# Kernel optimization log

Hardware: AMD Instinct MI355X
Metric: run time of the kernel (lower is better)

## Reference

```python
import jax, jax.numpy as jnp
import numpy as np

N = 10000
E = 256000
MUL = 32            # multiplicity per l (hidden_sizes = [32]*4)
NB = 10             # nbasis_funcs
RMAX = 3.5          # max_radius
NAVG = 25.6         # navg_neighbors
NGRAPH = 16         # number of graphs in batch
SLICES = [(0, 1), (1, 4), (4, 9), (9, 16)]  # l=0..3 blocks of the 16-dim SH rep


def _sph_harm(u):
    """Real spherical harmonics l=0..3, component normalization, on unit vectors. [E,16]"""
    x, y, z = u[:, 0], u[:, 1], u[:, 2]
    one = jnp.ones_like(x)
    s3 = 3.0 ** 0.5
    s15 = 15.0 ** 0.5
    s5 = 5.0 ** 0.5
    a = (35.0 / 8.0) ** 0.5
    b = 105.0 ** 0.5
    c = (21.0 / 8.0) ** 0.5
    d = 7.0 ** 0.5 / 2.0
    cols = [
        one,
        s3 * x, s3 * y, s3 * z,
        s15 * x * y, s15 * y * z, 0.5 * s5 * (3 * z * z - 1), s15 * x * z, 0.5 * s15 * (x * x - y * y),
        a * y * (3 * x * x - y * y), b * x * y * z, c * y * (5 * z * z - 1), d * z * (5 * z * z - 3),
        c * x * (5 * z * z - 1), 0.5 * b * z * (x * x - y * y), a * x * (x * x - 3 * y * y),
    ]
    return jnp.stack(cols, axis=1)


def _radial(emb, W1, W2):
    # FullyConnectedNet-style MLP with fan-in normalization and silu
    h = jax.nn.silu(emb @ W1 / (NB ** 0.5))
    return h @ W2 / (W1.shape[1] ** 0.5)


def _edge_geometry(pos, edge_src, edge_dst):
    vec = pos[edge_src] - pos[edge_dst]          # [E,3]
    r = jnp.linalg.norm(vec, axis=1)             # [E]
    u = vec / (r[:, None] + 1e-9)
    sh = _sph_harm(u)                            # [E,16]
    t = jnp.clip(r / RMAX, 0.0, 1.0)
    cutoff = jnp.where(r < RMAX, 0.5 * (jnp.cos(jnp.pi * t) + 1.0), 0.0)
    edge_attr = cutoff[:, None] * sh             # [E,16]
    centers = jnp.linspace(0.0, RMAX, NB)
    step = RMAX / (NB - 1)
    emb = jnp.exp(-(((r[:, None] - centers) / step) ** 2)) / 1.12 * (NB ** 0.5)
    return edge_attr, emb


def _layer(feat, edge_src, edge_dst, edge_attr, emb, Wsc, Wr1, Wr2):
    """Gated interaction block: self-connection + per-edge radial-weighted TP conv + gate."""
    n = feat.shape[0]
    # self-connection: per-l channel mixing
    sc = jnp.concatenate(
        [jnp.einsum('nci,co->noi', feat[:, :, a:b], Wsc[l]) for l, (a, b) in enumerate(SLICES)],
        axis=2) / (MUL ** 0.5)
    # per-edge weights from radial MLP: [E, 2 paths, 4 l's, MUL]
    w = _radial(emb, Wr1, Wr2).reshape(-1, 2, 4, MUL)
    xs = feat[edge_src]                          # [E,MUL,16] gather
    # path A (0e x Yl -> l) for l=0, plus path B (l x Yl -> 0e) for l=1..3 -> scalar slot
    scal = w[:, 0, 0, :] * xs[:, :, 0] * edge_attr[:, 0:1]
    parts = []
    for l, (a, b) in enumerate(SLICES):
        if l == 0:
            continue
        scal = scal + w[:, 1, l, :] * jnp.einsum('eci,ei->ec', xs[:, :, a:b], edge_attr[:, a:b])
        parts.append(w[:, 0, l, :, None] * xs[:, :, 0:1] * edge_attr[:, None, a:b])
    msg = jnp.concatenate([scal[:, :, None]] + parts, axis=2)   # [E,MUL,16]
    agg = jax.ops.segment_sum(msg, edge_dst, num_segments=n) / (NAVG ** 0.5)
    y = sc + agg
    # equivariant gate: silu on scalars, sigmoid(scalar) gates l>0 features
    s = y[:, :, 0]
    return jnp.concatenate(
        [jax.nn.silu(s)[:, :, None], y[:, :, 1:] * jax.nn.sigmoid(s)[:, :, None]], axis=2)


def _forward(pos, x, batch, edge_src, edge_dst, W_sc, Wr1, Wr2, Wf1, Wf2):
    n = pos.shape[0]
    edge_attr, emb = _edge_geometry(pos, edge_src, edge_dst)
    # lift scalar input features into the full l=0..3 layout
    feat = jnp.zeros((n, MUL, 16), x.dtype).at[:, :, 0].set(x)
    for i in range(3):
        feat = _layer(feat, edge_src, edge_dst, edge_attr, emb, W_sc[i], Wr1[i], Wr2[i])
    # final interaction block -> 1x0e output per node
    wf = _radial(emb, Wf1, Wf2).reshape(-1, 4, MUL)             # [E,4,MUL]
    xs = feat[edge_src]
    ms = wf[:, 0, :] * xs[:, :, 0] * edge_attr[:, 0:1]
    for l, (a, b) in enumerate(SLICES):
        if l == 0:
            continue
        ms = ms + wf[:, l, :] * jnp.einsum('eci,ei->ec', xs[:, :, a:b], edge_attr[:, a:b])
    node = jax.ops.segment_sum(ms.sum(axis=1) / (MUL ** 0.5), edge_dst, num_segments=n) / (NAVG ** 0.5)
    out = jax.ops.segment_sum(node, batch, num_segments=NGRAPH) / (NAVG ** 0.5)
    return out.flatten()


def setup_inputs() -> dict:
    key = jax.random.key(0)
    ks = jax.random.split(key, 10)
    pos = jax.random.uniform(ks[0], (N, 3), jnp.float32) * 5.0
    x = jax.random.normal(ks[1], (N, MUL), jnp.float32)
    batch = jnp.sort(jax.random.randint(ks[2], (N,), 0, NGRAPH, jnp.int32))
    edge_src = jax.random.randint(ks[3], (E,), 0, N, jnp.int32)
    edge_dst = jax.random.randint(ks[4], (E,), 0, N, jnp.int32)
    W_sc = jax.random.normal(ks[5], (3, 4, MUL, MUL), jnp.float32)
    Wr1 = jax.random.normal(ks[6], (3, NB, 64), jnp.float32)
    Wr2 = jax.random.normal(ks[7], (3, 64, 2 * 4 * MUL), jnp.float32)
    Wf1 = jax.random.normal(ks[8], (NB, 64), jnp.float32)
    Wf2 = jax.random.normal(ks[9], (64, 4 * MUL), jnp.float32)
    return {"pos": pos, "x": x, "batch": batch, "edge_src": edge_src, "edge_dst": edge_dst,
            "W_sc": W_sc, "Wr1": Wr1, "Wr2": Wr2, "Wf1": Wf1, "Wf2": Wf2}


def reference(pos, x, batch, edge_src, edge_dst, W_sc, Wr1, Wr2, Wf1, Wf2):
    return _forward(pos, x, batch, edge_src, edge_dst, W_sc, Wr1, Wr2, Wf1, Wf2)
```

## Files before the change

kernel.cpp:

```cpp
#include <hip/hip_runtime.h>
#include <math.h>

#define NN 10000
#define EE 256000
#define NGR 16
#define ECAP 150016

#define RSQRT10F   0.31622776601683794f
#define EMB_SCALE  2.8234621965789103f
#define INV_SQRT_MUL  0.17677669529663687f
#define INV_SQRT_NAVG 0.19764235376052372f
#define SCREC      (0.125f * INV_SQRT_NAVG)
#define STEPF      0.3888888888888889f
#define INV_STEPF  2.5714285714285716f
#define PIF        3.14159265358979323846f

__device__ __forceinline__ float sigm(float x) {
    return 1.0f / (1.0f + __expf(-x));
}

__device__ __forceinline__ void atomAddF(float* p, float v) {
    __hip_atomic_fetch_add(p, v, __ATOMIC_RELAXED, __HIP_MEMORY_SCOPE_AGENT);
}

__global__ __launch_bounds__(256) void count_kernel(
    const float* __restrict__ pos, const int* __restrict__ esrc,
    const int* __restrict__ edst, int* __restrict__ deg)
{
    int e = blockIdx.x * 256 + threadIdx.x;
    if (e >= EE) return;
    int s = esrc[e], d = edst[e];
    float vx = pos[3*s+0] - pos[3*d+0];
    float vy = pos[3*s+1] - pos[3*d+1];
    float vz = pos[3*s+2] - pos[3*d+2];
    float r2 = vx*vx + vy*vy + vz*vz;
    if (r2 < 12.25f) atomicAdd(&deg[d], 1);
}

__global__ __launch_bounds__(256) void scan_kernel(
    const int* __restrict__ deg, int* __restrict__ off, int* __restrict__ cursor)
{
    __shared__ int sbuf[256];
    const int t = threadIdx.x;
    const int start = t * 40;
    const int end = (start + 40 < NN) ? start + 40 : NN;
    int s = 0;
    for (int i = start; i < end; ++i) s += deg[i];
    sbuf[t] = s;
    __syncthreads();
    for (int d = 1; d < 256; d <<= 1) {
        int v = (t >= d) ? sbuf[t - d] : 0;
        __syncthreads();
        sbuf[t] += v;
        __syncthreads();
    }
    int run = sbuf[t] - s;
    for (int i = start; i < end; ++i) {
        off[i] = run; cursor[i] = run; run += deg[i];
    }
    if (t == 255) off[NN] = sbuf[255];
}

__global__ __launch_bounds__(256) void w1t_kernel(
    const float* __restrict__ Wr1, const float* __restrict__ Wf1,
    float* __restrict__ w1t)
{
    int t = blockIdx.x * 256 + threadIdx.x;
    if (t >= 4096) return;
    int i = t & 15;
    int j = (t >> 4) & 63;
    int l = t >> 10;
    float v;
    if (l < 3) v = (i < 10) ? Wr1[l * 640 + i * 64 + j] : 0.0f;
    else       v = (i < 10) ? Wf1[i * 64 + j] : 0.0f;
    w1t[l * 1024 + j * 16 + i] = v;
}

__global__ __launch_bounds__(256) void pack_kernel(
    const float* __restrict__ Wr2, const float* __restrict__ Wf2,
    float* __restrict__ wr2p, float* __restrict__ wf2p)
{
    const int offs[7] = {0, 32, 64, 96, 160, 192, 224};
    int t = blockIdx.x * 256 + threadIdx.x;
    if (t < 49152) {
        int k = t & 63;
        int j = (t >> 6) & 63;
        int g = (t >> 12) & 3;
        int layer = t >> 14;
        float v = 0.0f;
        if (k < 56)
            v = Wr2[layer * 16384 + j * 256 + offs[k >> 3] + g * 8 + (k & 7)];
        wr2p[t] = v;
    } else if (t < 49152 + 8192) {
        int t2 = t - 49152;
        int u = t2 & 15;
        int l = (t2 >> 4) & 3;
        int j = (t2 >> 6) & 63;
        int g = t2 >> 12;
        wf2p[t2] = Wf2[j * 128 + l * 32 + g * 16 + u];
    }
}

__global__ __launch_bounds__(256) void scatter_kernel(
    const float* __restrict__ pos, const int* __restrict__ esrc,
    const int* __restrict__ edst, int* __restrict__ cursor,
    int* __restrict__ csrc, int* __restrict__ cdst,
    float* __restrict__ attr_soa, float* __restrict__ attr_e,
    float* __restrict__ emb_soa)
{
    int e = blockIdx.x * 256 + threadIdx.x;
    if (e >= EE) return;
    int s = esrc[e], d = edst[e];
    float vx = pos[3*s+0] - pos[3*d+0];
    float vy = pos[3*s+1] - pos[3*d+1];
    float vz = pos[3*s+2] - pos[3*d+2];
    float r2 = vx*vx + vy*vy + vz*vz;
    if (r2 >= 12.25f) return;
    float r = sqrtf(r2);
    int slot = atomicAdd(&cursor[d], 1);
    if (slot >= ECAP) return;

    float inv = 1.0f / (r + 1e-9f);
    float x = vx * inv, y = vy * inv, z = vz * inv;

    float t = r * (1.0f / 3.5f);
    float cw = 0.5f * (cosf(PIF * t) + 1.0f);

    const float s3  = 1.7320508075688772f;
    const float s15 = 3.872983346207417f;
    const float s5  = 2.23606797749979f;
    const float a4  = 2.0916500663351889f;
    const float b4  = 10.246950765959598f;
    const float c4  = 1.6201851746019651f;
    const float d4  = 1.3228756555322954f;
    float xx = x*x, yy = y*y, zz = z*z;
    float sh[16];
    sh[0]  = 1.0f;
    sh[1]  = s3 * x;
    sh[2]  = s3 * y;
    sh[3]  = s3 * z;
    sh[4]  = s15 * x * y;
    sh[5]  = s15 * y * z;
    sh[6]  = 0.5f * s5 * (3.0f*zz - 1.0f);
    sh[7]  = s15 * x * z;
    sh[8]  = 0.5f * s15 * (xx - yy);
    sh[9]  = a4 * y * (3.0f*xx - yy);
    sh[10] = b4 * x * y * z;
    sh[11] = c4 * y * (5.0f*zz - 1.0f);
    sh[12] = d4 * z * (5.0f*zz - 3.0f);
    sh[13] = c4 * x * (5.0f*zz - 1.0f);
    sh[14] = 0.5f * b4 * z * (xx - yy);
    sh[15] = a4 * x * (xx - 3.0f*yy);

    float4* ae = (float4*)(attr_e + (size_t)slot * 16);
    #pragma unroll
    for (int q = 0; q < 4; ++q)
        ae[q] = make_float4(cw*sh[q*4], cw*sh[q*4+1], cw*sh[q*4+2], cw*sh[q*4+3]);

    #pragma unroll
    for (int i = 0; i < 16; ++i)
        attr_soa[(size_t)i * ECAP + slot] = cw * sh[i];
    #pragma unroll
    for (int k = 0; k < 10; ++k) {
        float dd = (r - (float)k * STEPF) * INV_STEPF;
        emb_soa[(size_t)k * ECAP + slot] = __expf(-dd * dd) * EMB_SCALE;
    }
    csrc[slot] = s;
    cdst[slot] = d;
}

__global__ __launch_bounds__(256) void init_feat_kernel(
    const float* __restrict__ x, float* __restrict__ feat)
{
    int t = blockIdx.x * 256 + threadIdx.x;
    if (t >= NN * 512) return;
    int i = t & 15;
    int c = (t >> 4) & 31;
    int n = t >> 9;
    feat[t] = (i == 0) ? x[n * 32 + c] : 0.0f;
}

__global__ __launch_bounds__(256) void h_kernel(
    const float* __restrict__ w1t, const float* __restrict__ emb_soa,
    float* __restrict__ h_soa, const int* __restrict__ cntp)
{
    const int tid = threadIdx.x;
    int cnt = *cntp; if (cnt > ECAP) cnt = ECAP;
    if (cnt == 0) return;
    const int e = blockIdx.x * 256 + tid;
    if (blockIdx.x * 256 >= cnt) return;
    const bool alive = (e < cnt);
    const int ee = alive ? e : (cnt - 1);

    float emb[10];
    #pragma unroll
    for (int i = 0; i < 10; ++i)
        emb[i] = emb_soa[(size_t)i * ECAP + ee];

    #pragma unroll 4
    for (int j = 0; j < 64; ++j) {
        const float* wj = w1t + j * 16;
        float a = 0.0f;
        #pragma unroll
        for (int i = 0; i < 10; ++i)
            a += emb[i] * wj[i];
        a *= RSQRT10F;
        if (alive)
            h_soa[(size_t)j * ECAP + e] = a * sigm(a);
    }
}

__global__ __launch_bounds__(256, 4) void edge_mlp_kernel(
    const float* __restrict__ wr2p, const float* __restrict__ h_soa,
    const float* __restrict__ fin, float* __restrict__ rec,
    const int* __restrict__ csrc,
    const float* __restrict__ attr_soa, const int* __restrict__ cntp)
{
    const int tid = threadIdx.x;
    const int g = blockIdx.y;
    const int c0 = g * 8;
    int cnt = *cntp; if (cnt > ECAP) cnt = ECAP;
    if (cnt == 0) return;
    const int e = blockIdx.x * 256 + tid;
    if (blockIdx.x * 256 >= cnt) return;
    const bool alive = (e < cnt);
    const int ee = alive ? e : (cnt - 1);

    float attr[16];
    #pragma unroll
    for (int i = 0; i < 16; ++i)
        attr[i] = attr_soa[(size_t)i * ECAP + ee];

    const float* xb = fin + (size_t)csrc[ee] * 512;
    const float* hp = h_soa + ee;
    const float* wg = wr2p + (size_t)g * 4096;
    float4* rec4 = (float4*)rec;

    float a0[8], a1[8], a2[8], a3[8], a4[8], a5[8], a6[8];
    #pragma unroll
    for (int u = 0; u < 8; ++u) {
        a0[u] = 0.f; a1[u] = 0.f; a2[u] = 0.f; a3[u] = 0.f;
        a4[u] = 0.f; a5[u] = 0.f; a6[u] = 0.f;
    }
    #pragma unroll 4
    for (int j = 0; j < 64; ++j) {
        const float hj = hp[(size_t)j * ECAP];
        const float* w = wg + j * 64;
        #pragma unroll
        for (int u = 0; u < 8; ++u) {
            a0[u] += hj * w[u];
            a1[u] += hj * w[8 + u];
            a2[u] += hj * w[16 + u];
            a3[u] += hj * w[24 + u];
            a4[u] += hj * w[32 + u];
            a5[u] += hj * w[40 + u];
            a6[u] += hj * w[48 + u];
        }
    }
    #pragma unroll
    for (int u = 0; u < 8; ++u) {
        const int c = c0 + u;
        const float4* xv = (const float4*)(xb + c * 16);
        float4 x0 = xv[0], x1 = xv[1], x2 = xv[2], x3 = xv[3];
        float d1 = x0.y*attr[1] + x0.z*attr[2] + x0.w*attr[3];
        float d2 = x1.x*attr[4] + x1.y*attr[5] + x1.z*attr[6]
                 + x1.w*attr[7] + x2.x*attr[8];
        float d3 = x2.y*attr[9] + x2.z*attr[10] + x2.w*attr[11]
                 + x3.x*attr[12] + x3.y*attr[13] + x3.z*attr[14]
                 + x3.w*attr[15];
        const float xs0 = x0.x;
        float scal = SCREC * (a0[u]*xs0*attr[0] + a4[u]*d1 + a5[u]*d2 + a6[u]*d3);
        float px = SCREC * xs0;
        if (alive)
            rec4[(size_t)c * ECAP + e] =
                make_float4(scal, a1[u] * px, a2[u] * px, a3[u] * px);
    }
}

__global__ __launch_bounds__(256) void agg_kernel(
    const float* __restrict__ fin, float* __restrict__ fout,
    const float* __restrict__ Wsc, const float* __restrict__ rec,
    const float* __restrict__ attr_e, const int* __restrict__ off)
{
    int t = blockIdx.x * 256 + threadIdx.x;
    int c = t & 31;
    int n = t >> 5;
    if (n >= NN) return;

    float acc[16];
    #pragma unroll
    for (int i = 0; i < 16; ++i) acc[i] = 0.0f;

    const float* f = fin + (size_t)n * 512;
    for (int cin = 0; cin < 32; ++cin) {
        float w0 = Wsc[          cin * 32 + c];
        float w1 = Wsc[1024 + cin * 32 + c];
        float w2 = Wsc[2048 + cin * 32 + c];
        float w3 = Wsc[3072 + cin * 32 + c];
        const float4* fv = (const float4*)(f + cin * 16);
        float4 f0 = fv[0], f1 = fv[1], f2 = fv[2], f3 = fv[3];
        acc[0]  += f0.x * w0;
        acc[1]  += f0.y * w1; acc[2]  += f0.z * w1; acc[3]  += f0.w * w1;
        acc[4]  += f1.x * w2; acc[5]  += f1.y * w2; acc[6]  += f1.z * w2;
        acc[7]  += f1.w * w2; acc[8]  += f2.x * w2;
        acc[9]  += f2.y * w3; acc[10] += f2.z * w3; acc[11] += f2.w * w3;
        acc[12] += f3.x * w3; acc[13] += f3.y * w3; acc[14] += f3.z * w3;
        acc[15] += f3.w * w3;
    }
    #pragma unroll
    for (int i = 0; i < 16; ++i) acc[i] *= INV_SQRT_MUL;

    const float4* rec4 = (const float4*)rec;
    int e0 = off[n], e1 = off[n + 1];
    if (e1 > ECAP) e1 = ECAP;
    for (int e = e0; e < e1; ++e) {
        float4 v = rec4[(size_t)c * ECAP + e];
        const float4* av = (const float4*)(attr_e + (size_t)e * 16);
        float4 A0 = av[0], A1 = av[1], A2 = av[2], A3 = av[3];
        acc[0]  += v.x;
        acc[1]  += v.y * A0.y;
        acc[2]  += v.y * A0.z;
        acc[3]  += v.y * A0.w;
        acc[4]  += v.z * A1.x;
        acc[5]  += v.z * A1.y;
        acc[6]  += v.z * A1.z;
        acc[7]  += v.z * A1.w;
        acc[8]  += v.z * A2.x;
        acc[9]  += v.w * A2.y;
        acc[10] += v.w * A2.z;
        acc[11] += v.w * A2.w;
        acc[12] += v.w * A3.x;
        acc[13] += v.w * A3.y;
        acc[14] += v.w * A3.z;
        acc[15] += v.w * A3.w;
    }

    float s = acc[0];
    float g = sigm(s);
    float4 o0 = make_float4(s * g,      acc[1] * g,  acc[2] * g,  acc[3] * g);
    float4 o1 = make_float4(acc[4] * g, acc[5] * g,  acc[6] * g,  acc[7] * g);
    float4 o2 = make_float4(acc[8] * g, acc[9] * g,  acc[10] * g, acc[11] * g);
    float4 o3 = make_float4(acc[12] * g, acc[13] * g, acc[14] * g, acc[15] * g);
    float4* ov = (float4*)(fout + (size_t)n * 512 + c * 16);
    ov[0] = o0; ov[1] = o1; ov[2] = o2; ov[3] = o3;
}

__global__ __launch_bounds__(256, 2) void final_edge_kernel(
    const float* __restrict__ wf2p, const float* __restrict__ h_soa,
    const float* __restrict__ fin, float* __restrict__ fbuf,
    const int* __restrict__ csrc,
    const float* __restrict__ attr_soa, const int* __restrict__ cntp)
{
    const int tid = threadIdx.x;
    const int g = blockIdx.y;
    const int c0 = g * 16;
    int cnt = *cntp; if (cnt > ECAP) cnt = ECAP;
    if (cnt == 0) return;
    const int e = blockIdx.x * 256 + tid;
    if (blockIdx.x * 256 >= cnt) return;
    const bool alive = (e < cnt);
    const int ee = alive ? e : (cnt - 1);

    float attr[16];
    #pragma unroll
    for (int i = 0; i < 16; ++i)
        attr[i] = attr_soa[(size_t)i * ECAP + ee];

    const float* hp = h_soa + ee;
    const float* wg = wf2p + (size_t)g * 4096;
    float H0[16], H1[16], H2[16], H3[16];
    #pragma unroll
    for (int u = 0; u < 16; ++u) { H0[u]=0.f; H1[u]=0.f; H2[u]=0.f; H3[u]=0.f; }
    #pragma unroll 2
    for (int j = 0; j < 64; ++j) {
        const float hj = hp[(size_t)j * ECAP];
        const float* w = wg + j * 64;
        #pragma unroll
        for (int u = 0; u < 16; ++u) {
            H0[u] += hj * w[u];
            H1[u] += hj * w[16 + u];
            H2[u] += hj * w[32 + u];
            H3[u] += hj * w[48 + u];
        }
    }

    const float* xb = fin + (size_t)csrc[ee] * 512;
    float msum = 0.0f;
    #pragma unroll 2
    for (int u = 0; u < 16; ++u) {
        const float4* xv = (const float4*)(xb + (c0 + u) * 16);
        float4 x0 = xv[0], x1 = xv[1], x2 = xv[2], x3 = xv[3];
        float d0 = x0.x * attr[0];
        float d1 = x0.y*attr[1] + x0.z*attr[2] + x0.w*attr[3];
        float d2 = x1.x*attr[4] + x1.y*attr[5] + x1.z*attr[6]
                 + x1.w*attr[7] + x2.x*attr[8];
        float d3 = x2.y*attr[9] + x2.z*attr[10] + x2.w*attr[11]
                 + x3.x*attr[12] + x3.y*attr[13] + x3.z*attr[14]
                 + x3.w*attr[15];
        msum += H0[u]*d0 + H1[u]*d1 + H2[u]*d2 + H3[u]*d3;
    }

    if (alive)
        fbuf[(size_t)g * ECAP + e] = msum * 0.125f;
}

__global__ __launch_bounds__(256) void out_kernel(
    const float* __restrict__ fbuf, const int* __restrict__ off,
    const int* __restrict__ batch, float* __restrict__ out)
{
    __shared__ float bins[NGR];
    int t = blockIdx.x * 256 + threadIdx.x;
    if (threadIdx.x < NGR) bins[threadIdx.x] = 0.0f;
    __syncthreads();
    if (t < NN) {
        int e0 = off[t], e1 = off[t + 1];
        if (e1 > ECAP) e1 = ECAP;
        float s = 0.0f;
        for (int e = e0; e < e1; ++e)
            s += fbuf[e] + fbuf[(size_t)ECAP + e];
        atomicAdd(&bins[batch[t]], s * (INV_SQRT_MUL * (1.0f / 25.6f)));
    }
    __syncthreads();
    if (threadIdx.x < NGR) atomAddF(out + threadIdx.x, bins[threadIdx.x]);
}

extern "C" void kernel_launch(void* const* d_in, const int* in_sizes, int n_in,
                              void* d_out, int out_size, void* d_ws, size_t ws_size,
                              hipStream_t stream)
{
    const float* pos  = (const float*)d_in[0];
    const float* x    = (const float*)d_in[1];
    const int*   batch= (const int*)  d_in[2];
    const int*   esrc = (const int*)  d_in[3];
    const int*   edst = (const int*)  d_in[4];
    const float* W_sc = (const float*)d_in[5];
    const float* Wr1  = (const float*)d_in[6];
    const float* Wr2  = (const float*)d_in[7];
    const float* Wf1  = (const float*)d_in[8];
    const float* Wf2  = (const float*)d_in[9];
    float* out = (float*)d_out;

    char* ws = (char*)d_ws;
    size_t off_b = 0;
    auto alloc = [&](size_t bytes) -> void* {
        void* p = ws + off_b;
        off_b = (off_b + bytes + 255) & ~(size_t)255;
        return p;
    };
    int*   deg      = (int*)  alloc((size_t)NN * 4);
    int*   off      = (int*)  alloc((size_t)(NN + 1) * 4);
    int*   cursor   = (int*)  alloc((size_t)NN * 4);
    int*   csrc     = (int*)  alloc((size_t)ECAP * 4);
    int*   cdst     = (int*)  alloc((size_t)ECAP * 4);
    float* w1t      = (float*)alloc((size_t)4 * 1024 * 4);
    float* wr2p     = (float*)alloc((size_t)3 * 16384 * 4);
    float* wf2p     = (float*)alloc((size_t)8192 * 4);
    float* emb_soa  = (float*)alloc((size_t)10 * ECAP * 4);
    float* attr_soa = (float*)alloc((size_t)16 * ECAP * 4);
    float* attr_e   = (float*)alloc((size_t)16 * ECAP * 4);
    float* h_soa    = (float*)alloc((size_t)64 * ECAP * 4);
    float* rec      = (float*)alloc((size_t)128 * ECAP * 4);
    float* feat_a   = (float*)alloc((size_t)NN * 512 * 4);
    float* feat_b   = (float*)alloc((size_t)NN * 512 * 4);

    hipMemsetAsync(deg, 0, (size_t)NN * 4, stream);
    hipMemsetAsync(d_out, 0, (size_t)out_size * 4, stream);

    count_kernel<<<(EE + 255) / 256, 256, 0, stream>>>(pos, esrc, edst, deg);
    scan_kernel<<<1, 256, 0, stream>>>(deg, off, cursor);
    w1t_kernel<<<16, 256, 0, stream>>>(Wr1, Wf1, w1t);
    pack_kernel<<<(49152 + 8192 + 255) / 256, 256, 0, stream>>>(
        Wr2, Wf2, wr2p, wf2p);
    scatter_kernel<<<(EE + 255) / 256, 256, 0, stream>>>(
        pos, esrc, edst, cursor, csrc, cdst, attr_soa, attr_e, emb_soa);
    init_feat_kernel<<<(NN * 512 + 255) / 256, 256, 0, stream>>>(x, feat_a);

    const int* cntp = off + NN;
    float* fin = feat_a;
    float* fout = feat_b;
    dim3 egrid(ECAP / 256, 4);
    for (int layer = 0; layer < 3; ++layer) {
        h_kernel<<<ECAP / 256, 256, 0, stream>>>(
            w1t + layer * 1024, emb_soa, h_soa, cntp);
        edge_mlp_kernel<<<egrid, 256, 0, stream>>>(
            wr2p + (size_t)layer * 16384, h_soa, fin, rec,
            csrc, attr_soa, cntp);
        agg_kernel<<<(NN * 32 + 255) / 256, 256, 0, stream>>>(
            fin, fout, W_sc + layer * 4096, rec, attr_e, off);
        float* tmp = fin; fin = fout; fout = tmp;
    }
    h_kernel<<<ECAP / 256, 256, 0, stream>>>(
        w1t + 3 * 1024, emb_soa, h_soa, cntp);
    float* fbuf = rec;
    final_edge_kernel<<<dim3(ECAP / 256, 2), 256, 0, stream>>>(
        wf2p, h_soa, fin, fbuf, csrc, attr_soa, cntp);
    out_kernel<<<(NN + 255) / 256, 256, 0, stream>>>(fbuf, off, batch, out);
}
```

Before: 838.0 us.

## Store radial hidden per edge as rows and loop channel groups in one thread

The hidden activations h move from a structure-of-arrays layout to an edge-major layout of 64 floats per edge. h_kernel now writes each edge's values as float4 chunks, and the MLP kernels read them back with float4 loads. edge_mlp_kernel drops its 4-way blockIdx.y split over channel groups and loops over the 4 groups inside each thread, so h and attr are loaded once per edge instead of once per group. In exchange the grid has 4x fewer blocks and launch bounds drop to 2 blocks per CU. The per-thread float4 row reads are strided by 256 bytes, which makes loads less coalesced than the old SoA layout.

```diff
diff --git a/kernel.cpp b/kernel.cpp
--- a/kernel.cpp
+++ b/kernel.cpp
@@ -182,7 +182,7 @@
 
 __global__ __launch_bounds__(256) void h_kernel(
     const float* __restrict__ w1t, const float* __restrict__ emb_soa,
-    float* __restrict__ h_soa, const int* __restrict__ cntp)
+    float* __restrict__ h_e, const int* __restrict__ cntp)
 {
     const int tid = threadIdx.x;
     int cnt = *cntp; if (cnt > ECAP) cnt = ECAP;
@@ -197,28 +197,33 @@
     for (int i = 0; i < 10; ++i)
         emb[i] = emb_soa[(size_t)i * ECAP + ee];
 
+    float4* hrow = (float4*)(h_e + (size_t)e * 64);
     #pragma unroll 4
-    for (int j = 0; j < 64; ++j) {
-        const float* wj = w1t + j * 16;
-        float a = 0.0f;
+    for (int jb = 0; jb < 16; ++jb) {
+        float hv[4];
         #pragma unroll
-        for (int i = 0; i < 10; ++i)
-            a += emb[i] * wj[i];
-        a *= RSQRT10F;
+        for (int q = 0; q < 4; ++q) {
+            const int j = jb * 4 + q;
+            const float* wj = w1t + j * 16;
+            float a = 0.0f;
+            #pragma unroll
+            for (int i = 0; i < 10; ++i)
+                a += emb[i] * wj[i];
+            a *= RSQRT10F;
+            hv[q] = a * sigm(a);
+        }
         if (alive)
-            h_soa[(size_t)j * ECAP + e] = a * sigm(a);
-    }
-}
-
-__global__ __launch_bounds__(256, 4) void edge_mlp_kernel(
-    const float* __restrict__ wr2p, const float* __restrict__ h_soa,
+            hrow[jb] = make_float4(hv[0], hv[1], hv[2], hv[3]);
+    }
+}
+
+__global__ __launch_bounds__(256, 2) void edge_mlp_kernel(
+    const float* __restrict__ wr2p, const float* __restrict__ h_e,
     const float* __restrict__ fin, float* __restrict__ rec,
     const int* __restrict__ csrc,
     const float* __restrict__ attr_soa, const int* __restrict__ cntp)
 {
     const int tid = threadIdx.x;
-    const int g = blockIdx.y;
-    const int c0 = g * 8;
     int cnt = *cntp; if (cnt > ECAP) cnt = ECAP;
     if (cnt == 0) return;
     const int e = blockIdx.x * 256 + tid;
@@ -232,48 +237,56 @@
         attr[i] = attr_soa[(size_t)i * ECAP + ee];
 
     const float* xb = fin + (size_t)csrc[ee] * 512;
-    const float* hp = h_soa + ee;
-    const float* wg = wr2p + (size_t)g * 4096;
+    const float4* hrow = (const float4*)(h_e + (size_t)ee * 64);
     float4* rec4 = (float4*)rec;
 
-    float a0[8], a1[8], a2[8], a3[8], a4[8], a5[8], a6[8];
-    #pragma unroll
-    for (int u = 0; u < 8; ++u) {
-        a0[u] = 0.f; a1[u] = 0.f; a2[u] = 0.f; a3[u] = 0.f;
-        a4[u] = 0.f; a5[u] = 0.f; a6[u] = 0.f;
-    }
-    #pragma unroll 4
-    for (int j = 0; j < 64; ++j) {
-        const float hj = hp[(size_t)j * ECAP];
-        const float* w = wg + j * 64;
+    for (int g = 0; g < 4; ++g) {
+        const float* wg = wr2p + (size_t)g * 4096;
+        float a0[8], a1[8], a2[8], a3[8], a4[8], a5[8], a6[8];
         #pragma unroll
         for (int u = 0; u < 8; ++u) {
-            a0[u] += hj * w[u];
-            a1[u] += hj * w[8 + u];
-            a2[u] += hj * w[16 + u];
-            a3[u] += hj * w[24 + u];
-            a4[u] += hj * w[32 + u];
-            a5[u] += hj * w[40 + u];
-            a6[u] += hj * w[48 + u];
+            a0[u] = 0.f; a1[u] = 0.f; a2[u] = 0.f; a3[u] = 0.f;
+            a4[u] = 0.f; a5[u] = 0.f; a6[u] = 0.f;
         }
-    }
-    #pragma unroll
-    for (int u = 0; u < 8; ++u) {
-        const int c = c0 + u;
-        const float4* xv = (const float4*)(xb + c * 16);
-        float4 x0 = xv[0], x1 = xv[1], x2 = xv[2], x3 = xv[3];
-        float d1 = x0.y*attr[1] + x0.z*attr[2] + x0.w*attr[3];
-        float d2 = x1.x*attr[4] + x1.y*attr[5] + x1.z*attr[6]
-                 + x1.w*attr[7] + x2.x*attr[8];
-        float d3 = x2.y*attr[9] + x2.z*attr[10] + x2.w*attr[11]
-                 + x3.x*attr[12] + x3.y*attr[13] + x3.z*attr[14]
-                 + x3.w*attr[15];
-        const float xs0 = x0.x;
-        float scal = SCREC * (a0[u]*xs0*attr[0] + a4[u]*d1 + a5[u]*d2 + a6[u]*d3);
-        float px = SCREC * xs0;
-        if (alive)
-            rec4[(size_t)c * ECAP + e] =
-                make_float4(scal, a1[u] * px, a2[u] * px, a3[u] * px);
+        #pragma unroll 2
+        for (int jb = 0; jb < 16; ++jb) {
+            const float4 hv = hrow[jb];
+            #pragma unroll
+            for (int q = 0; q < 4; ++q) {
+                const float hj = (q == 0) ? hv.x : (q == 1) ? hv.y
+                               : (q == 2) ? hv.z : hv.w;
+                const float* w = wg + (jb * 4 + q) * 64;
+                #pragma unroll
+                for (int u = 0; u < 8; ++u) {
+                    a0[u] += hj * w[u];
+                    a1[u] += hj * w[8 + u];
+                    a2[u] += hj * w[16 + u];
+                    a3[u] += hj * w[24 + u];
+                    a4[u] += hj * w[32 + u];
+                    a5[u] += hj * w[40 + u];
+                    a6[u] += hj * w[48 + u];
+                }
+            }
+        }
+        const int c0 = g * 8;
+        #pragma unroll
+        for (int u = 0; u < 8; ++u) {
+            const int c = c0 + u;
+            const float4* xv = (const float4*)(xb + c * 16);
+            float4 x0 = xv[0], x1 = xv[1], x2 = xv[2], x3 = xv[3];
+            float d1 = x0.y*attr[1] + x0.z*attr[2] + x0.w*attr[3];
+            float d2 = x1.x*attr[4] + x1.y*attr[5] + x1.z*attr[6]
+                     + x1.w*attr[7] + x2.x*attr[8];
+            float d3 = x2.y*attr[9] + x2.z*attr[10] + x2.w*attr[11]
+                     + x3.x*attr[12] + x3.y*attr[13] + x3.z*attr[14]
+                     + x3.w*attr[15];
+            const float xs0 = x0.x;
+            float scal = SCREC * (a0[u]*xs0*attr[0] + a4[u]*d1 + a5[u]*d2 + a6[u]*d3);
+            float px = SCREC * xs0;
+            if (alive)
+                rec4[(size_t)c * ECAP + e] =
+                    make_float4(scal, a1[u] * px, a2[u] * px, a3[u] * px);
+        }
     }
 }
 
@@ -346,7 +359,7 @@
 }
 
 __global__ __launch_bounds__(256, 2) void final_edge_kernel(
-    const float* __restrict__ wf2p, const float* __restrict__ h_soa,
+    const float* __restrict__ wf2p, const float* __restrict__ h_e,
     const float* __restrict__ fin, float* __restrict__ fbuf,
     const int* __restrict__ csrc,
     const float* __restrict__ attr_soa, const int* __restrict__ cntp)
@@ -366,21 +379,26 @@
     for (int i = 0; i < 16; ++i)
         attr[i] = attr_soa[(size_t)i * ECAP + ee];
 
-    const float* hp = h_soa + ee;
+    const float4* hrow = (const float4*)(h_e + (size_t)ee * 64);
     const float* wg = wf2p + (size_t)g * 4096;
     float H0[16], H1[16], H2[16], H3[16];
     #pragma unroll
     for (int u = 0; u < 16; ++u) { H0[u]=0.f; H1[u]=0.f; H2[u]=0.f; H3[u]=0.f; }
     #pragma unroll 2
-    for (int j = 0; j < 64; ++j) {
-        const float hj = hp[(size_t)j * ECAP];
-        const float* w = wg + j * 64;
+    for (int jb = 0; jb < 16; ++jb) {
+        const float4 hv = hrow[jb];
         #pragma unroll
-        for (int u = 0; u < 16; ++u) {
-            H0[u] += hj * w[u];
-            H1[u] += hj * w[16 + u];
-            H2[u] += hj * w[32 + u];
-            H3[u] += hj * w[48 + u];
+        for (int q = 0; q < 4; ++q) {
+            const float hj = (q == 0) ? hv.x : (q == 1) ? hv.y
+                           : (q == 2) ? hv.z : hv.w;
+            const float* w = wg + (jb * 4 + q) * 64;
+            #pragma unroll
+            for (int u = 0; u < 16; ++u) {
+                H0[u] += hj * w[u];
+                H1[u] += hj * w[16 + u];
+                H2[u] += hj * w[32 + u];
+                H3[u] += hj * w[48 + u];
+            }
         }
     }
 
@@ -458,7 +476,7 @@
     float* emb_soa  = (float*)alloc((size_t)10 * ECAP * 4);
     float* attr_soa = (float*)alloc((size_t)16 * ECAP * 4);
     float* attr_e   = (float*)alloc((size_t)16 * ECAP * 4);
-    float* h_soa    = (float*)alloc((size_t)64 * ECAP * 4);
+    float* h_e      = (float*)alloc((size_t)64 * ECAP * 4);
     float* rec      = (float*)alloc((size_t)128 * ECAP * 4);
     float* feat_a   = (float*)alloc((size_t)NN * 512 * 4);
     float* feat_b   = (float*)alloc((size_t)NN * 512 * 4);
@@ -478,21 +496,20 @@
     const int* cntp = off + NN;
     float* fin = feat_a;
     float* fout = feat_b;
-    dim3 egrid(ECAP / 256, 4);
     for (int layer = 0; layer < 3; ++layer) {
         h_kernel<<<ECAP / 256, 256, 0, stream>>>(
-            w1t + layer * 1024, emb_soa, h_soa, cntp);
-        edge_mlp_kernel<<<egrid, 256, 0, stream>>>(
-            wr2p + (size_t)layer * 16384, h_soa, fin, rec,
+            w1t + layer * 1024, emb_soa, h_e, cntp);
+        edge_mlp_kernel<<<ECAP / 256, 256, 0, stream>>>(
+            wr2p + (size_t)layer * 16384, h_e, fin, rec,
             csrc, attr_soa, cntp);
         agg_kernel<<<(NN * 32 + 255) / 256, 256, 0, stream>>>(
             fin, fout, W_sc + layer * 4096, rec, attr_e, off);
         float* tmp = fin; fin = fout; fout = tmp;
     }
     h_kernel<<<ECAP / 256, 256, 0, stream>>>(
-        w1t + 3 * 1024, emb_soa, h_soa, cntp);
+        w1t + 3 * 1024, emb_soa, h_e, cntp);
     float* fbuf = rec;
     final_edge_kernel<<<dim3(ECAP / 256, 2), 256, 0, stream>>>(
-        wf2p, h_soa, fin, fbuf, csrc, attr_soa, cntp);
+        wf2p, h_e, fin, fbuf, csrc, attr_soa, cntp);
     out_kernel<<<(NN + 255) / 256, 256, 0, stream>>>(fbuf, off, batch, out);
 }
```

New measurement: 1.755 ms. +109.4%, slower.
